# Kernel tuning notes

Measured on AMD Instinct MI355X. Metric: run time of the kernel, lower is better.

## Reference

```python
import jax, jax.numpy as jnp
import numpy as np
from jax import lax

TS = 64.0  # timestep_ in the original module


def get_spikes(x, th):
    # Integrate-and-fire with reset-by-subtraction (catCuda.getSpikes),
    # batched over all channels with per-channel thresholds.
    # x: [N,C,H,W,T], th: [C]
    thb = th[None, :, None, None]
    xT = jnp.moveaxis(x, -1, 0)  # [T,N,C,H,W]

    def step(v, xt):
        v = v + xt
        s = (v >= thb).astype(x.dtype)
        return v - s * thb, s

    _, sT = lax.scan(step, jnp.zeros_like(xT[0]), xT)
    return jnp.moveaxis(sT, 0, -1)  # [N,C,H,W,T]


def conv2d(x, w, b, pad):
    out = lax.conv_general_dilated(x, w, (1, 1), [(pad, pad), (pad, pad)],
                                   dimension_numbers=('NCHW', 'OIHW', 'NCHW'))
    return out + b[None, :, None, None]


def snn_conv(x, w, b, pad):
    # per-timestep 2D conv on [N,C,H,W,T]: fold T into batch
    N, C, H, W, T = x.shape
    xt = jnp.moveaxis(x, -1, 1).reshape(N * T, C, H, W)
    out = conv2d(xt, w, b, pad)
    Co, Ho, Wo = out.shape[1], out.shape[2], out.shape[3]
    return jnp.moveaxis(out.reshape(N, T, Co, Ho, Wo), 1, -1)


def avgpool2(y):
    N, C, H, W = y.shape
    return y.reshape(N, C, H // 2, 2, W // 2, 2).mean(axis=(3, 5))


def snn_pool(x):
    N, C, H, W, T = x.shape
    return x.reshape(N, C, H // 2, 2, W // 2, 2, T).mean(axis=(3, 5))


def tt(x5, y4, th):
    # threshold_training_snn: spikes from SNN pre-activation, quantized-clamped
    # ANN activation, and online per-channel threshold update.
    y_new = get_spikes(x5, th)
    y = jnp.clip(jnp.floor(y4 * TS) / TS, 0.0, 1.0)
    mul = x5.shape[0] * x5.shape[2] * x5.shape[3] * x5.shape[4]
    diff = (y.sum(axis=(0, 2, 3)) * TS - y_new.sum(axis=(0, 2, 3, 4))) / mul
    return y_new, y, th - 0.1 * diff


def setup_inputs():
    key = jax.random.key(0)
    ks = jax.random.split(key, 40)
    chans = [(3, 128), (128, 128), (128, 256), (256, 256), (256, 512), (512, 512), (512, 1024)]
    inp = {}
    for idx, (ci, co) in enumerate(chans):
        inp['w%ds' % (idx + 1)] = jax.random.normal(ks[2 * idx], (co, ci, 3, 3), jnp.float32) / np.float32(np.sqrt(ci * 9))
        inp['b%ds' % (idx + 1)] = jnp.zeros((co,), jnp.float32)
        inp['w%da' % (idx + 1)] = jax.random.normal(ks[2 * idx + 1], (co, ci, 3, 3), jnp.float32) / np.float32(np.sqrt(ci * 9))
        inp['b%da' % (idx + 1)] = jnp.zeros((co,), jnp.float32)
    inp['wc'] = jax.random.normal(ks[30], (100, 1024), jnp.float32) / 32.0
    inp['bc'] = jnp.zeros((100,), jnp.float32)
    inp['x'] = jax.random.uniform(ks[31], (4, 3, 32, 32, 64), jnp.float32)
    for name, c in [('threshold_pre_1', 128), ('threshold_pre_2', 128), ('threshold_pre_3', 256),
                    ('threshold_pre_4', 256), ('threshold_pre_5', 512), ('threshold_pre_6', 512),
                    ('threshold_pre_7', 1024), ('p1', 128), ('p2', 256), ('p3', 512), ('p4', 1024)]:
        inp[name] = jnp.ones((c,), jnp.float32)
    return inp


def reference(x, threshold_pre_1, threshold_pre_2, threshold_pre_3, threshold_pre_4,
              threshold_pre_5, threshold_pre_6, threshold_pre_7, p1, p2, p3, p4,
              w1s, b1s, w1a, b1a, w2s, b2s, w2a, b2a, w3s, b3s, w3a, b3a,
              w4s, b4s, w4a, b4a, w5s, b5s, w5a, b5a, w6s, b6s, w6a, b6a,
              w7s, b7s, w7a, b7a, wc, bc):
    x_ = x.sum(axis=-1) / TS
    xs, y, t1 = tt(snn_conv(x, w1s, b1s, 1), conv2d(x_, w1a, b1a, 1), threshold_pre_1)
    xs, y, t2 = tt(snn_conv(xs, w2s, b2s, 1), conv2d(y, w2a, b2a, 1), threshold_pre_2)
    xs, y, q1 = tt(snn_pool(xs), avgpool2(y), p1)
    xs, y, t3 = tt(snn_conv(xs, w3s, b3s, 1), conv2d(y, w3a, b3a, 1), threshold_pre_3)
    xs, y, t4 = tt(snn_conv(xs, w4s, b4s, 1), conv2d(y, w4a, b4a, 1), threshold_pre_4)
    xs, y, q2 = tt(snn_pool(xs), avgpool2(y), p2)
    xs, y, t5 = tt(snn_conv(xs, w5s, b5s, 1), conv2d(y, w5a, b5a, 1), threshold_pre_5)
    xs, y, t6 = tt(snn_conv(xs, w6s, b6s, 1), conv2d(y, w6a, b6a, 1), threshold_pre_6)
    xs, y, q3 = tt(snn_pool(xs), avgpool2(y), p3)
    xs, y, t7 = tt(snn_conv(xs, w7s, b7s, 0), conv2d(y, w7a, b7a, 0), threshold_pre_7)
    xs, y, q4 = tt(snn_pool(xs), avgpool2(y), p4)
    # classifier on [N,1024,1,1,T] spike trains, then sum over time / T
    logits_t = jnp.einsum('nct,oc->not', xs[:, :, 0, 0, :], wc) + bc[None, :, None]
    out = logits_t.sum(axis=-1) / TS
    return (out, t1, t2, t3, t4, t5, t6, t7, q1, q2, q3, q4)
```

## Files before the change

### kernel.cpp

```cpp
#include <hip/hip_runtime.h>
#include <cstdint>
#include <cstddef>


typedef short short8 __attribute__((ext_vector_type(8)));
typedef float floatx4 __attribute__((ext_vector_type(4)));

__device__ __forceinline__ unsigned short f2bf_rne(float f) {
  unsigned u = __float_as_uint(f);
  return (unsigned short)((u + 0x7FFFu + ((u >> 16) & 1u)) >> 16);
}
__device__ __forceinline__ float bf2f(unsigned short h) {
  return __uint_as_float((unsigned)h << 16);
}

__global__ __launch_bounds__(256) void k_wxform(const float* __restrict__ Wsrc,
                                                unsigned short* __restrict__ wt,
                                                int Ci, int Co) {
  const int nch = Ci >> 5;
  const int total = (Co >> 6) * nch * 9 * 4 * 64;
  int idx = blockIdx.x * 256 + threadIdx.x;
  if (idx >= total) return;
  int lane = idx & 63;
  int t2 = idx >> 6;
  int cg = t2 & 3;
  int t3 = t2 >> 2;
  int tap = t3 % 9;
  int t4 = t3 / 9;
  int ch = t4 % nch;
  int cot = t4 / nch;
  int co = cot * 64 + cg * 16 + (lane & 15);
  int cib = ch * 32 + (lane >> 4) * 8;
  short8 vh, vl;
  #pragma unroll
  for (int j = 0; j < 8; ++j) {
    float wv = Wsrc[((size_t)co * Ci + cib + j) * 9 + tap];
    unsigned short h = f2bf_rne(wv);
    vh[j] = (short)h;
    vl[j] = (short)f2bf_rne(wv - bf2f(h));
  }
  size_t base = ((((size_t)cot * nch + ch) * 9 + tap) * 4 + cg) * 1024 + (size_t)lane * 8;
  *(short8*)&wt[base] = vh;
  *(short8*)&wt[base + 512] = vl;
}

__global__ __launch_bounds__(256) void k_wxform1(const float* __restrict__ Wsrc,
                                                 unsigned short* __restrict__ wt) {
  int idx = blockIdx.x * 256 + threadIdx.x;
  if (idx >= 512) return;
  int lane = idx & 63, cg = (idx >> 6) & 3, cot = idx >> 8;
  int co = cot * 64 + cg * 16 + (lane & 15);
  short8 vh, vl;
  #pragma unroll
  for (int e = 0; e < 8; ++e) {
    int k = (lane >> 4) * 8 + e;
    float wv = 0.f;
    if (k < 27) { int tap = k / 3, ci = k - 3 * tap; wv = Wsrc[(co * 3 + ci) * 9 + tap]; }
    unsigned short h = f2bf_rne(wv);
    vh[e] = (short)h;
    vl[e] = (short)f2bf_rne(wv - bf2f(h));
  }
  size_t base = (size_t)cot * 4096 + cg * 1024 + (size_t)lane * 8;
  *(short8*)&wt[base] = vh;
  *(short8*)&wt[base + 512] = vl;
}

__global__ __launch_bounds__(256) void k_tpack(const float* __restrict__ x,
                                               unsigned* __restrict__ XT2) {
  int idx = blockIdx.x * 256 + threadIdx.x;
  int b = idx / 3072;
  int rem = idx - b * 3072;
  int t = b & 63, n = b >> 6;
  float f = x[((size_t)(n * 3072 + rem)) * 64 + t];
  unsigned short h = f2bf_rne(f);
  unsigned short l = f2bf_rne(f - bf2f(h));
  XT2[idx] = (unsigned)h | ((unsigned)l << 16);
}

__global__ __launch_bounds__(256) void k_xbar_pack(const float* __restrict__ x,
                                                   unsigned* __restrict__ xb) {
  int idx = blockIdx.x * 256 + threadIdx.x;
  if (idx >= 12288) return;
  const float* p = x + (size_t)idx * 64;
  float s = 0.f;
  #pragma unroll
  for (int t = 0; t < 64; ++t) s += p[t];
  s *= 0.015625f;
  unsigned short h = f2bf_rne(s);
  unsigned short l = f2bf_rne(s - bf2f(h));
  xb[idx] = (unsigned)h | ((unsigned)l << 16);
}

template <typename T, bool PAD0, int G, int KCH>
__global__ __launch_bounds__(256, 1) void k_cmfma(
    const T* __restrict__ in, const unsigned short* __restrict__ wt,
    const float* __restrict__ bs, float* __restrict__ out,
    int Ci, int Co, int W, int TRI, int tpi, int NIMG, int nImgValid,
    int nchPer, size_t osplit) {
  constexpr int MT = G * 16;
  constexpr int PPXMAX = PAD0 ? (MT / 4) * 16 : 208;
  constexpr int STR = KCH * 32 + 8;
  __shared__ unsigned short sIn[PPXMAX * STR];
  const int tid = threadIdx.x;
  const int lane = tid & 63;
  const int wv = tid >> 6;
  const int cot = blockIdx.x;
  const int mtile = blockIdx.y;
  const int kz = blockIdx.z;
  const int nch = Ci >> 5;
  const int nchA = kz * nchPer, nchB = nchA + nchPer;
  out += (size_t)kz * osplit;
  const int addBias = (kz == 0);

  int img_first, r0 = 0, PPR, PPX;
  if constexpr (PAD0) {
    img_first = mtile * (MT / 4);
    PPR = 16; PPX = (MT / 4) * 16;
  } else {
    img_first = (mtile / tpi) * NIMG;
    r0 = (mtile % tpi) * TRI;
    PPR = (TRI + 2) * (W + 2);
    PPX = NIMG * PPR;
  }
  const int TRW = TRI * W;

  int p0[G], mimg[G], mopx[G];
  #pragma unroll
  for (int g = 0; g < G; ++g) {
    int m = g * 16 + (lane & 15);
    int limg;
    if constexpr (PAD0) {
      limg = m >> 2;
      int o = m & 3;
      p0[g] = limg * 16 + (o >> 1) * 4 + (o & 1);
      mopx[g] = (o >> 1) * 2 + (o & 1);
    } else {
      limg = m / TRW;
      int rm = m - limg * TRW;
      int r = rm / W, c = rm - r * W;
      p0[g] = limg * PPR + r * (W + 2) + c;
      mopx[g] = (r0 + r) * W + c;
    }
    mimg[g] = img_first + limg;
  }
  int psh[9];
  #pragma unroll
  for (int t = 0; t < 9; ++t) {
    int dh = t / 3, dw = t - dh * 3;
    psh[t] = PAD0 ? (dh * 4 + dw) : (dh * (W + 2) + dw);
  }

  const int HWin = PAD0 ? 16 : W * W;
  int sgofs[2]; bool svalid[2];
  #pragma unroll
  for (int i = 0; i < 2; ++i) {
    int p = tid + i * 256;
    svalid[i] = false; sgofs[i] = 0;
    if (p < PPX) {
      int limg, gpx;
      if constexpr (PAD0) {
        limg = p >> 4; gpx = p & 15;
      } else {
        limg = p / PPR;
        int rem = p - limg * PPR;
        int pr = rem / (W + 2), pc = rem - pr * (W + 2);
        int gr = r0 + pr - 1, gc = pc - 1;
        gpx = (gr >= 0 && gr < W && gc >= 0 && gc < W) ? gr * W + gc : -1;
      }
      int img = img_first + limg;
      if (gpx >= 0 && img < nImgValid) {
        svalid[i] = true;
        sgofs[i] = img * Ci * HWin + gpx;
      }
    }
  }
  const int kb = (lane >> 4) * 8;

  floatx4 acc[G];
  floatx4 zero = {0.f, 0.f, 0.f, 0.f};
  #pragma unroll
  for (int g = 0; g < G; ++g) acc[g] = zero;

  for (int c2 = nchA; c2 < nchB; ++c2) {
    const int ci0 = c2 * (KCH * 32);
    #pragma unroll
    for (int i = 0; i < 2; ++i) {
      int p = tid + i * 256;
      if (p < PPX) {
        unsigned short* dst = &sIn[p * STR];
        if (svalid[i]) {
          const T* sp = in + sgofs[i] + (size_t)ci0 * HWin;
          #pragma unroll
          for (int j = 0; j < KCH * 4; ++j) {
            short8 v;
            #pragma unroll
            for (int e = 0; e < 8; ++e) {
              if constexpr (sizeof(T) == 1)
                v[e] = sp[(size_t)(j * 8 + e) * HWin] ? (short)0x3F80 : (short)0;
              else
                v[e] = (short)f2bf_rne(((const float*)sp)[(size_t)(j * 8 + e) * HWin]);
            }
            *(short8*)&dst[j * 8] = v;
          }
        } else {
          short8 z = {};
          #pragma unroll
          for (int j = 0; j < KCH * 4; ++j) *(short8*)&dst[j * 8] = z;
        }
      }
    }
    __syncthreads();
    const unsigned short* wbase = wt + ((size_t)(cot * nch + c2 * KCH)) * 36864
                                  + (size_t)wv * 1024 + (size_t)lane * 8;
    constexpr int ST = 9 * KCH;
    short8 A[2][2];
    A[0][0] = *(const short8*)(wbase);
    A[0][1] = *(const short8*)(wbase + 512);
    #pragma unroll
    for (int st = 0; st < ST; ++st) {
      const int cur = st & 1;
      if (st + 1 < ST) {
        const int s1 = (st + 1) / 9, t1 = (st + 1) % 9;
        const unsigned short* wp = wbase + (size_t)s1 * 36864 + (size_t)t1 * 4096;
        A[cur ^ 1][0] = *(const short8*)(wp);
        A[cur ^ 1][1] = *(const short8*)(wp + 512);
      }
      const int s = st / 9, tap = st % 9;
      short8 b[G];
      #pragma unroll
      for (int g = 0; g < G; ++g)
        b[g] = *(const short8*)&sIn[(p0[g] + psh[tap]) * STR + s * 32 + kb];
      #pragma unroll
      for (int g = 0; g < G; ++g) {
        acc[g] = __builtin_amdgcn_mfma_f32_16x16x32_bf16(A[cur][0], b[g], acc[g], 0, 0, 0);
        acc[g] = __builtin_amdgcn_mfma_f32_16x16x32_bf16(A[cur][1], b[g], acc[g], 0, 0, 0);
      }
    }
    __syncthreads();
  }
  const int HWout = PAD0 ? 4 : W * W;
  #pragma unroll
  for (int g = 0; g < G; ++g) {
    if (mimg[g] >= nImgValid) continue;
    #pragma unroll
    for (int i2 = 0; i2 < 4; ++i2) {
      int co = cot * 64 + wv * 16 + (lane >> 4) * 4 + i2;
      float bv = addBias ? bs[co] : 0.f;
      out[((size_t)mimg[g] * Co + co) * HWout + mopx[g]] = acc[g][i2] + bv;
    }
  }
}

__global__ __launch_bounds__(256, 1) void k_l1(const unsigned* __restrict__ xin,
                                               const unsigned short* __restrict__ wt,
                                               const float* __restrict__ bs,
                                               float* __restrict__ out,
                                               int nImgValid) {
  __shared__ unsigned short sIn[256 * 72];
  const int tid = threadIdx.x, lane = tid & 63, wv = tid >> 6;
  const int cot = blockIdx.x, mtile = blockIdx.y;
  const int img = mtile >> 2;
  const int r0 = (mtile & 3) * 8;
  {
    int m = tid;
    int r = r0 + (m >> 5), c = m & 31;
    const unsigned* ip = xin + (size_t)img * 3072;
    unsigned v[9][3];
    bool iv = (img < nImgValid);
    #pragma unroll
    for (int dh = 0; dh < 3; ++dh) {
      #pragma unroll
      for (int dw = 0; dw < 3; ++dw) {
        int rr = r + dh - 1, cc = c + dw - 1;
        bool ok = iv && rr >= 0 && rr < 32 && cc >= 0 && cc < 32;
        #pragma unroll
        for (int ci = 0; ci < 3; ++ci)
          v[dh * 3 + dw][ci] = ok ? ip[ci * 1024 + rr * 32 + cc] : 0u;
      }
    }
    #pragma unroll
    for (int j = 0; j < 4; ++j) {
      short8 vh, vl;
      #pragma unroll
      for (int e = 0; e < 8; ++e) {
        int k = j * 8 + e;
        unsigned u = (k < 27) ? v[k / 3][k - 3 * (k / 3)] : 0u;
        vh[e] = (short)(u & 0xFFFFu);
        vl[e] = (short)(u >> 16);
      }
      *(short8*)&sIn[m * 72 + j * 8] = vh;
      *(short8*)&sIn[m * 72 + 32 + j * 8] = vl;
    }
  }
  __syncthreads();
  const int kb = (lane >> 4) * 8;
  const unsigned short* wb = wt + (size_t)cot * 4096 + (size_t)lane * 8;
  short8 Af[8];
  #pragma unroll
  for (int f = 0; f < 8; ++f)
    Af[f] = *(const short8*)(wb + (f >> 1) * 1024 + (f & 1) * 512);
  floatx4 acc[4][4];
  floatx4 zero = {0.f, 0.f, 0.f, 0.f};
  #pragma unroll
  for (int cg = 0; cg < 4; ++cg)
    #pragma unroll
    for (int g = 0; g < 4; ++g) acc[cg][g] = zero;
  short8 bh[4], bl[4];
  #pragma unroll
  for (int g = 0; g < 4; ++g) {
    int m = wv * 64 + g * 16 + (lane & 15);
    bh[g] = *(const short8*)&sIn[m * 72 + kb];
    bl[g] = *(const short8*)&sIn[m * 72 + 32 + kb];
  }
  #pragma unroll
  for (int cg = 0; cg < 4; ++cg) {
    #pragma unroll
    for (int g = 0; g < 4; ++g) {
      acc[cg][g] = __builtin_amdgcn_mfma_f32_16x16x32_bf16(Af[cg * 2 + 0], bh[g], acc[cg][g], 0, 0, 0);
      acc[cg][g] = __builtin_amdgcn_mfma_f32_16x16x32_bf16(Af[cg * 2 + 0], bl[g], acc[cg][g], 0, 0, 0);
      acc[cg][g] = __builtin_amdgcn_mfma_f32_16x16x32_bf16(Af[cg * 2 + 1], bh[g], acc[cg][g], 0, 0, 0);
    }
  }
  if (img >= nImgValid) return;
  #pragma unroll
  for (int g = 0; g < 4; ++g) {
    int mbase = wv * 64 + g * 16 + (lane & 15);
    int px = (r0 + (mbase >> 5)) * 32 + (mbase & 31);
    #pragma unroll
    for (int cg = 0; cg < 4; ++cg) {
      #pragma unroll
      for (int i2 = 0; i2 < 4; ++i2) {
        int co = cot * 64 + cg * 16 + (lane >> 4) * 4 + i2;
        out[((size_t)img * 128 + co) * 1024 + px] = acc[cg][g][i2] + bs[co];
      }
    }
  }
}

__global__ __launch_bounds__(256) void k_if(const float* __restrict__ X,
                                            uint8_t* __restrict__ Sp,
                                            const float* __restrict__ th,
                                            float* __restrict__ ssum,
                                            int C, int HW,
                                            int nparts, size_t pstride) {
  const int CHW = C * HW;
  int idx = blockIdx.x * 256 + threadIdx.x;
  if (idx >= CHW) return;
  int c = idx / HW;
  const float thv = th[c];
  size_t base = (size_t)blockIdx.y * 64 * CHW + idx;
  const float* p = X + base;
  uint8_t* q = Sp + base;
  float v = 0.f, ss = 0.f;
  #pragma unroll
  for (int t = 0; t < 64; ++t) {
    const float* pt = p + (size_t)t * CHW;
    float xv = pt[0];
    for (int u = 1; u < nparts; ++u) xv += pt[(size_t)u * pstride];
    v += xv;
    float s = (v >= thv) ? 1.f : 0.f;
    v -= s * thv;
    q[(size_t)t * CHW] = (uint8_t)s;
    ss += s;
  }
  if ((HW & 63) == 0) {
    for (int off = 32; off >= 1; off >>= 1) ss += __shfl_down(ss, off);
    if ((threadIdx.x & 63) == 0) atomicAdd(&ssum[c], ss);
  } else {
    atomicAdd(&ssum[c], ss);
  }
}

__global__ __launch_bounds__(256) void k_ifpool(const uint8_t* __restrict__ Sin,
                                                uint8_t* __restrict__ Sp,
                                                const float* __restrict__ th,
                                                float* __restrict__ ssum,
                                                float* __restrict__ Sout,
                                                int C, int H) {
  const int Ho = H >> 1, HWo = Ho * Ho;
  const int CHWo = C * HWo;
  int idx = blockIdx.x * 256 + threadIdx.x;
  if (idx >= CHWo) return;
  int c = idx / HWo;
  int rem = idx - c * HWo;
  int ho = rem / Ho, wo = rem - ho * Ho;
  const float thv = th[c];
  const size_t istep = (size_t)C * H * H;
  const size_t ib = ((size_t)(blockIdx.y * 64) * C + c) * (H * H) + (2 * ho) * H + 2 * wo;
  uint8_t* q = Sp + (size_t)blockIdx.y * 64 * CHWo + idx;
  float v = 0.f, ss = 0.f;
  #pragma unroll
  for (int t = 0; t < 64; ++t) {
    const uint8_t* pp = Sin + ib + (size_t)t * istep;
    float xv = 0.25f * ((float)pp[0] + (float)pp[1] + (float)pp[H] + (float)pp[H + 1]);
    v += xv;
    float s = (v >= thv) ? 1.f : 0.f;
    v -= s * thv;
    q[(size_t)t * CHWo] = (uint8_t)s;
    ss += s;
  }
  if (Sout && HWo == 1) Sout[blockIdx.y * C + c] = ss;
  if ((HWo & 63) == 0) {
    for (int off = 32; off >= 1; off >>= 1) ss += __shfl_down(ss, off);
    if ((threadIdx.x & 63) == 0) atomicAdd(&ssum[c], ss);
  } else {
    atomicAdd(&ssum[c], ss);
  }
}

__global__ __launch_bounds__(256) void k_ttypool(const float* __restrict__ yin,
                                                 float* __restrict__ yout,
                                                 float* __restrict__ ysum,
                                                 int C, int H) {
  const int Ho = H >> 1, HWo = Ho * Ho;
  int idx = blockIdx.x * 256 + threadIdx.x;
  if (idx >= 4 * C * HWo) return;
  int rem = idx % (C * HWo);
  int c = rem / HWo;
  int r2 = rem - c * HWo;
  int ho = r2 / Ho, wo = r2 - ho * Ho;
  int img = idx / (C * HWo);
  size_t base = (((size_t)img * C + c) * H + 2 * ho) * H + 2 * wo;
  float xv = 0.25f * (yin[base] + yin[base + 1] + yin[base + H] + yin[base + H + 1]);
  float v = floorf(xv * 64.f) * 0.015625f;
  v = fminf(fmaxf(v, 0.f), 1.f);
  yout[idx] = v;
  if ((HWo & 63) == 0) {
    for (int off = 32; off >= 1; off >>= 1) v += __shfl_down(v, off);
    if ((threadIdx.x & 63) == 0) atomicAdd(&ysum[c], v);
  } else {
    atomicAdd(&ysum[c], v);
  }
}

__global__ __launch_bounds__(256) void k_tty(const float* __restrict__ y4,
                                             float* __restrict__ yout,
                                             float* __restrict__ ysum,
                                             int C, int HW,
                                             int nparts, int pstride) {
  int idx = blockIdx.x * 256 + threadIdx.x;
  if (idx >= 4 * C * HW) return;
  int rem = idx % (C * HW);
  int c = rem / HW;
  float xv = 0.f;
  for (int p = 0; p < nparts; ++p) xv += y4[idx + (size_t)p * pstride];
  float v = floorf(xv * 64.f) * 0.015625f;
  v = fminf(fmaxf(v, 0.f), 1.f);
  yout[idx] = v;
  if ((HW & 63) == 0) {
    for (int off = 32; off >= 1; off >>= 1) v += __shfl_down(v, off);
    if ((threadIdx.x & 63) == 0) atomicAdd(&ysum[c], v);
  } else {
    atomicAdd(&ysum[c], v);
  }
}

__global__ void k_thr(const float* __restrict__ thin,
                      const float* __restrict__ ssum,
                      const float* __restrict__ ysum,
                      float* __restrict__ dst, int C, float invmul) {
  int c = blockIdx.x * 256 + threadIdx.x;
  if (c >= C) return;
  float diff = (ysum[c] * 64.f - ssum[c]) * invmul;
  dst[c] = thin[c] - 0.1f * diff;
}

__global__ void k_cls(const float* __restrict__ S, const float* __restrict__ wc,
                      const float* __restrict__ bcp, float* __restrict__ out) {
  int idx = blockIdx.x * 256 + threadIdx.x;
  if (idx >= 400) return;
  int n = idx / 100, o = idx - (idx / 100) * 100;
  const float* sp = S + n * 1024;
  const float* wp = wc + o * 1024;
  float acc = 0.f;
  for (int c = 0; c < 1024; ++c) acc += wp[c] * sp[c];
  out[idx] = acc * 0.015625f + bcp[o];
}

extern "C" void kernel_launch(void* const* d_in, const int* in_sizes, int n_in,
                              void* d_out_v, int out_size, void* d_ws, size_t ws_size,
                              hipStream_t stream) {
  const float *Ws[7], *Bs[7], *Wa[7], *Ba[7];
  for (int i = 0; i < 7; ++i) {
    Ws[i] = (const float*)d_in[i * 4 + 0];
    Bs[i] = (const float*)d_in[i * 4 + 1];
    Wa[i] = (const float*)d_in[i * 4 + 2];
    Ba[i] = (const float*)d_in[i * 4 + 3];
  }
  const float* wc = (const float*)d_in[28];
  const float* bc = (const float*)d_in[29];
  const float* x  = (const float*)d_in[30];
  const float* TH[7];
  for (int i = 0; i < 7; ++i) TH[i] = (const float*)d_in[31 + i];
  const float* P[4];
  for (int i = 0; i < 4; ++i) P[i] = (const float*)d_in[38 + i];
  float* out = (float*)d_out_v;

  float* w = (float*)d_ws;
  const size_t RF = 8536064;
  float* Rb = w;
  size_t off = RF;
  float* xbar = w + off; off += 12288;
  float* yA   = w + off; off += 524288;
  float* yB   = w + off; off += 524288;
  float* y4   = w + off; off += 524288;
  float* S    = w + off; off += 4096;
  float* sums = w + off; off += 11 * 2048;
  uint8_t* SA = (uint8_t*)(w + off);
  uint8_t* SB = SA + 33554432;
  size_t total_bytes = off * sizeof(float) + (size_t)2 * 33554432;
  if (ws_size < total_bytes) return;
  unsigned short* WT = (unsigned short*)Rb;
  unsigned* XT2 = (unsigned*)SB;
  unsigned* xbar2 = (unsigned*)xbar;

  hipMemsetAsync(sums, 0, 11 * 2048 * sizeof(float), stream);
  k_tpack<<<3072, 256, 0, stream>>>(x, XT2);
  k_xbar_pack<<<48, 256, 0, stream>>>(x, xbar2);

  int stage = 0;

  {
    float* CF = Rb + 4096;
    float* ss = sums; float* ys = ss + 1024;
    k_wxform1<<<2, 256, 0, stream>>>(Ws[0], WT);
    for (int c = 0; c < 4; ++c) {
      k_l1<<<dim3(2, 256), 256, 0, stream>>>(XT2 + (size_t)c * 64 * 3072, WT, Bs[0], CF, 64);
      k_if<<<dim3(512, 1), 256, 0, stream>>>(CF, SA + (size_t)c * 64 * 131072,
                                             TH[0], ss, 128, 1024, 1, 0);
    }
    k_wxform1<<<2, 256, 0, stream>>>(Wa[0], WT);
    k_l1<<<dim3(2, 16), 256, 0, stream>>>(xbar2, WT, Ba[0], y4, 4);
    k_tty<<<2048, 256, 0, stream>>>(y4, yA, ys, 128, 1024, 1, 0);
    k_thr<<<1, 256, 0, stream>>>(TH[0], ss, ys, out + 400, 128, 1.0f / (4.f * 1024.f * 64.f));
    ++stage;
  }

  auto mfma_layer = [&](const uint8_t* inS, uint8_t* outS, const float* inY, float* outY,
                        int li, int Ci, int Co, int W, int TRI, int tpi, int NIMG,
                        int chunkImgs, int kzn, float* CF1,
                        int aTRI, int atpi, int akz,
                        const float* thin, int outoff) {
    const int HW = W * W;
    const int CHWo = Co * HW;
    const int nch = Ci >> 5;
    float* ss = sums + stage * 2048; float* ys = ss + 1024;
    float* CF = Rb + (size_t)Co * Ci * 9;
    size_t osplit = (kzn == 2) ? (size_t)(CF1 - CF) : 0;
    int xgrid = ((Co / 64) * nch * 9 * 4 * 64 + 255) / 256;
    k_wxform<<<xgrid, 256, 0, stream>>>(Ws[li], WT, Ci, Co);
    int nchk = 256 / chunkImgs;
    int mt = (chunkImgs / NIMG) * tpi;
    for (int c = 0; c < nchk; ++c) {
      k_cmfma<uint8_t, false, 8, 1><<<dim3(Co / 64, mt, kzn), 256, 0, stream>>>(
          inS + (size_t)c * chunkImgs * Ci * HW, WT, Bs[li], CF,
          Ci, Co, W, TRI, tpi, NIMG, chunkImgs, nch / kzn, osplit);
      k_if<<<dim3((CHWo + 255) / 256, chunkImgs / 64), 256, 0, stream>>>(
          CF, outS + (size_t)c * chunkImgs * CHWo, thin, ss, Co, HW, kzn, osplit);
    }
    k_wxform<<<xgrid, 256, 0, stream>>>(Wa[li], WT, Ci, Co);
    int aosplit = 4 * CHWo;
    k_cmfma<float, false, 4, 1><<<dim3(Co / 64, 4 * atpi, akz), 256, 0, stream>>>(
        inY, WT, Ba[li], y4, Ci, Co, W, aTRI, atpi, 1, 4, nch / akz, (size_t)aosplit);
    k_tty<<<(4 * CHWo + 255) / 256, 256, 0, stream>>>(y4, outY, ys, Co, HW, akz, aosplit);
    k_thr<<<(Co + 255) / 256, 256, 0, stream>>>(thin, ss, ys, out + outoff, Co,
                                                1.0f / (4.f * HW * 64.f));
    ++stage;
  };

  auto pool_stage = [&](const uint8_t* inS, uint8_t* outS, const float* inY, float* outY,
                        int C, int H, const float* pthr, int outoff, float* Sout) {
    const int Ho = H / 2, HWo = Ho * Ho;
    const int CHWo = C * HWo;
    float* ss = sums + stage * 2048; float* ys = ss + 1024;
    k_ifpool<<<dim3((CHWo + 255) / 256, 4), 256, 0, stream>>>(inS, outS, pthr, ss, Sout, C, H);
    k_ttypool<<<(4 * CHWo + 255) / 256, 256, 0, stream>>>(inY, outY, ys, C, H);
    k_thr<<<(C + 255) / 256, 256, 0, stream>>>(pthr, ss, ys, out + outoff, C,
                                               1.0f / (4.f * HWo * 64.f));
    ++stage;
  };

  mfma_layer(SA, SB, yA, yB, 1, 128, 128, 32, 4, 8, 1, 64, 1, nullptr,
             2, 16, 1, TH[1], 528);
  pool_stage(SB, SA, yB, yA, 128, 32, P[0], 3216, nullptr);
  mfma_layer(SA, SB, yA, yB, 2, 128, 256, 16, 8, 2, 1, 64, 2,
             (float*)(SB + 16777216), 4, 4, 2, TH[2], 656);
  mfma_layer(SB, SA, yB, yA, 3, 256, 256, 16, 8, 2, 1, 64, 2,
             (float*)(SA + 16777216), 4, 4, 2, TH[3], 912);
  pool_stage(SA, SB, yA, yB, 256, 16, P[1], 3344, nullptr);
  mfma_layer(SB, SA, yB, yA, 4, 256, 512, 8, 8, 1, 2, 128, 2,
             (float*)(SA + 8388608), 8, 1, 4, TH[4], 1168);
  mfma_layer(SA, SB, yA, yB, 5, 512, 512, 8, 8, 1, 2, 128, 2,
             (float*)(SB + 8388608), 8, 1, 4, TH[5], 1680);
  pool_stage(SB, SA, yB, yA, 512, 8, P[2], 3600, nullptr);
  {
    float* ss = sums + stage * 2048; float* ys = ss + 1024;
    float* CF = (float*)(SA + 4194304);
    const size_t osplit = 1048576;
    int xgrid = (16 * 16 * 9 * 4 * 64 + 255) / 256;
    k_wxform<<<xgrid, 256, 0, stream>>>(Ws[6], WT, 512, 1024);
    k_cmfma<uint8_t, true, 8, 1><<<dim3(16, 8, 4), 256, 0, stream>>>(
        SA, WT, Bs[6], CF, 512, 1024, 4, 0, 1, 0, 256, 4, osplit);
    k_if<<<dim3(16, 4), 256, 0, stream>>>(CF, SB, TH[6], ss, 1024, 4, 4, osplit);
    k_wxform<<<xgrid, 256, 0, stream>>>(Wa[6], WT, 512, 1024);
    k_cmfma<float, true, 4, 1><<<dim3(16, 1, 8), 256, 0, stream>>>(
        yA, WT, Ba[6], y4, 512, 1024, 4, 0, 1, 0, 4, 2, 16384);
    k_tty<<<64, 256, 0, stream>>>(y4, yB, ys, 1024, 4, 8, 16384);
    k_thr<<<4, 256, 0, stream>>>(TH[6], ss, ys, out + 2192, 1024, 1.0f / 1024.f);
    ++stage;
  }
  pool_stage(SB, SA, yB, yA, 1024, 2, P[3], 4112, S);
  k_cls<<<2, 256, 0, stream>>>(S, wc, bc, out);
}
```

Measured before the change: 1.999 ms.

## Register-block spike conv MFMA over two output-channel groups per wave

Reworks the MFMA conv kernel so each wave computes two 16-channel output groups over a pixel sub-tile. This doubles the block's pixel tile to 256 and reuses each LDS B fragment across two A fragments. The KCH channel-chunking parameter is dropped. Spike-path layer launch parameters (rows per tile, images per tile) are retuned so the new tile sizes fit. The aim is fewer LDS reads per MFMA and fewer redundant weight loads, at the cost of more accumulator registers and half as many blocks per launch.

Measured after the change: 1.801 ms, median of 2. -9.9%, faster.

```diff
diff --git a/kernel.cpp b/kernel.cpp
--- a/kernel.cpp
+++ b/kernel.cpp
@@ -91,19 +91,22 @@
   xb[idx] = (unsigned)h | ((unsigned)l << 16);
 }
 
-template <typename T, bool PAD0, int G, int KCH>
+template <typename T, bool PAD0, int GW, int NPG>
 __global__ __launch_bounds__(256, 1) void k_cmfma(
     const T* __restrict__ in, const unsigned short* __restrict__ wt,
     const float* __restrict__ bs, float* __restrict__ out,
     int Ci, int Co, int W, int TRI, int tpi, int NIMG, int nImgValid,
     int nchPer, size_t osplit) {
-  constexpr int MT = G * 16;
-  constexpr int PPXMAX = PAD0 ? (MT / 4) * 16 : 208;
-  constexpr int STR = KCH * 32 + 8;
+  constexpr int CW = NPG;
+  constexpr int MT = 16 * GW * NPG;
+  constexpr int PPXMAX = PAD0 ? (MT / 4) * 16 : 400;
+  constexpr int STR = 40;
   __shared__ unsigned short sIn[PPXMAX * STR];
   const int tid = threadIdx.x;
   const int lane = tid & 63;
   const int wv = tid >> 6;
+  const int cog = wv / NPG;
+  const int pxg = wv % NPG;
   const int cot = blockIdx.x;
   const int mtile = blockIdx.y;
   const int kz = blockIdx.z;
@@ -124,10 +127,10 @@
   }
   const int TRW = TRI * W;
 
-  int p0[G], mimg[G], mopx[G];
-  #pragma unroll
-  for (int g = 0; g < G; ++g) {
-    int m = g * 16 + (lane & 15);
+  int p0[GW], mimg[GW], mopx[GW];
+  #pragma unroll
+  for (int g = 0; g < GW; ++g) {
+    int m = pxg * (GW * 16) + g * 16 + (lane & 15);
     int limg;
     if constexpr (PAD0) {
       limg = m >> 2;
@@ -176,13 +179,15 @@
   }
   const int kb = (lane >> 4) * 8;
 
-  floatx4 acc[G];
+  floatx4 acc[CW][GW];
   floatx4 zero = {0.f, 0.f, 0.f, 0.f};
   #pragma unroll
-  for (int g = 0; g < G; ++g) acc[g] = zero;
-
-  for (int c2 = nchA; c2 < nchB; ++c2) {
-    const int ci0 = c2 * (KCH * 32);
+  for (int cw = 0; cw < CW; ++cw)
+    #pragma unroll
+    for (int g = 0; g < GW; ++g) acc[cw][g] = zero;
+
+  for (int ch = nchA; ch < nchB; ++ch) {
+    const int ci0 = ch * 32;
     #pragma unroll
     for (int i = 0; i < 2; ++i) {
       int p = tid + i * 256;
@@ -191,7 +196,7 @@
         if (svalid[i]) {
           const T* sp = in + sgofs[i] + (size_t)ci0 * HWin;
           #pragma unroll
-          for (int j = 0; j < KCH * 4; ++j) {
+          for (int j = 0; j < 4; ++j) {
             short8 v;
             #pragma unroll
             for (int e = 0; e < 8; ++e) {
@@ -205,48 +210,57 @@
         } else {
           short8 z = {};
           #pragma unroll
-          for (int j = 0; j < KCH * 4; ++j) *(short8*)&dst[j * 8] = z;
+          for (int j = 0; j < 4; ++j) *(short8*)&dst[j * 8] = z;
         }
       }
     }
     __syncthreads();
-    const unsigned short* wbase = wt + ((size_t)(cot * nch + c2 * KCH)) * 36864
-                                  + (size_t)wv * 1024 + (size_t)lane * 8;
-    constexpr int ST = 9 * KCH;
-    short8 A[2][2];
-    A[0][0] = *(const short8*)(wbase);
-    A[0][1] = *(const short8*)(wbase + 512);
-    #pragma unroll
-    for (int st = 0; st < ST; ++st) {
-      const int cur = st & 1;
-      if (st + 1 < ST) {
-        const int s1 = (st + 1) / 9, t1 = (st + 1) % 9;
-        const unsigned short* wp = wbase + (size_t)s1 * 36864 + (size_t)t1 * 4096;
-        A[cur ^ 1][0] = *(const short8*)(wp);
-        A[cur ^ 1][1] = *(const short8*)(wp + 512);
-      }
-      const int s = st / 9, tap = st % 9;
-      short8 b[G];
+    const unsigned short* wbase = wt + ((size_t)(cot * nch + ch)) * 36864
+                                  + (size_t)(cog * CW) * 1024 + (size_t)lane * 8;
+    short8 A[2][CW * 2];
+    #pragma unroll
+    for (int cw = 0; cw < CW; ++cw) {
+      A[0][cw * 2 + 0] = *(const short8*)(wbase + cw * 1024);
+      A[0][cw * 2 + 1] = *(const short8*)(wbase + cw * 1024 + 512);
+    }
+    #pragma unroll
+    for (int t = 0; t < 9; ++t) {
+      const int cur = t & 1;
+      if (t < 8) {
+        const unsigned short* wp = wbase + (size_t)(t + 1) * 4096;
+        #pragma unroll
+        for (int cw = 0; cw < CW; ++cw) {
+          A[cur ^ 1][cw * 2 + 0] = *(const short8*)(wp + cw * 1024);
+          A[cur ^ 1][cw * 2 + 1] = *(const short8*)(wp + cw * 1024 + 512);
+        }
+      }
+      short8 b[GW];
       #pragma unroll
-      for (int g = 0; g < G; ++g)
-        b[g] = *(const short8*)&sIn[(p0[g] + psh[tap]) * STR + s * 32 + kb];
+      for (int g = 0; g < GW; ++g)
+        b[g] = *(const short8*)&sIn[(p0[g] + psh[t]) * STR + kb];
       #pragma unroll
-      for (int g = 0; g < G; ++g) {
-        acc[g] = __builtin_amdgcn_mfma_f32_16x16x32_bf16(A[cur][0], b[g], acc[g], 0, 0, 0);
-        acc[g] = __builtin_amdgcn_mfma_f32_16x16x32_bf16(A[cur][1], b[g], acc[g], 0, 0, 0);
+      for (int cw = 0; cw < CW; ++cw) {
+        #pragma unroll
+        for (int g = 0; g < GW; ++g) {
+          acc[cw][g] = __builtin_amdgcn_mfma_f32_16x16x32_bf16(A[cur][cw * 2 + 0], b[g], acc[cw][g], 0, 0, 0);
+          acc[cw][g] = __builtin_amdgcn_mfma_f32_16x16x32_bf16(A[cur][cw * 2 + 1], b[g], acc[cw][g], 0, 0, 0);
+        }
       }
     }
     __syncthreads();
   }
   const int HWout = PAD0 ? 4 : W * W;
   #pragma unroll
-  for (int g = 0; g < G; ++g) {
+  for (int g = 0; g < GW; ++g) {
     if (mimg[g] >= nImgValid) continue;
     #pragma unroll
-    for (int i2 = 0; i2 < 4; ++i2) {
-      int co = cot * 64 + wv * 16 + (lane >> 4) * 4 + i2;
-      float bv = addBias ? bs[co] : 0.f;
-      out[((size_t)mimg[g] * Co + co) * HWout + mopx[g]] = acc[g][i2] + bv;
+    for (int cw = 0; cw < CW; ++cw) {
+      #pragma unroll
+      for (int i2 = 0; i2 < 4; ++i2) {
+        int co = cot * 64 + (cog * CW + cw) * 16 + (lane >> 4) * 4 + i2;
+        float bv = addBias ? bs[co] : 0.f;
+        out[((size_t)mimg[g] * Co + co) * HWout + mopx[g]] = acc[cw][g][i2] + bv;
+      }
     }
   }
 }
@@ -552,7 +566,7 @@
     int nchk = 256 / chunkImgs;
     int mt = (chunkImgs / NIMG) * tpi;
     for (int c = 0; c < nchk; ++c) {
-      k_cmfma<uint8_t, false, 8, 1><<<dim3(Co / 64, mt, kzn), 256, 0, stream>>>(
+      k_cmfma<uint8_t, false, 8, 2><<<dim3(Co / 64, mt, kzn), 256, 0, stream>>>(
           inS + (size_t)c * chunkImgs * Ci * HW, WT, Bs[li], CF,
           Ci, Co, W, TRI, tpi, NIMG, chunkImgs, nch / kzn, osplit);
       k_if<<<dim3((CHWo + 255) / 256, chunkImgs / 64), 256, 0, stream>>>(
@@ -580,17 +594,17 @@
     ++stage;
   };
 
-  mfma_layer(SA, SB, yA, yB, 1, 128, 128, 32, 4, 8, 1, 64, 1, nullptr,
+  mfma_layer(SA, SB, yA, yB, 1, 128, 128, 32, 8, 4, 1, 64, 1, nullptr,
              2, 16, 1, TH[1], 528);
   pool_stage(SB, SA, yB, yA, 128, 32, P[0], 3216, nullptr);
-  mfma_layer(SA, SB, yA, yB, 2, 128, 256, 16, 8, 2, 1, 64, 2,
+  mfma_layer(SA, SB, yA, yB, 2, 128, 256, 16, 16, 1, 1, 64, 2,
              (float*)(SB + 16777216), 4, 4, 2, TH[2], 656);
-  mfma_layer(SB, SA, yB, yA, 3, 256, 256, 16, 8, 2, 1, 64, 2,
+  mfma_layer(SB, SA, yB, yA, 3, 256, 256, 16, 16, 1, 1, 64, 2,
              (float*)(SA + 16777216), 4, 4, 2, TH[3], 912);
   pool_stage(SA, SB, yA, yB, 256, 16, P[1], 3344, nullptr);
-  mfma_layer(SB, SA, yB, yA, 4, 256, 512, 8, 8, 1, 2, 128, 2,
+  mfma_layer(SB, SA, yB, yA, 4, 256, 512, 8, 8, 1, 4, 128, 2,
              (float*)(SA + 8388608), 8, 1, 4, TH[4], 1168);
-  mfma_layer(SA, SB, yA, yB, 5, 512, 512, 8, 8, 1, 2, 128, 2,
+  mfma_layer(SA, SB, yA, yB, 5, 512, 512, 8, 8, 1, 4, 128, 2,
              (float*)(SB + 8388608), 8, 1, 4, TH[5], 1680);
   pool_stage(SB, SA, yB, yA, 512, 8, P[2], 3600, nullptr);
   {
```
